# Optimization experiments

Hardware: AMD Instinct MI355X
Metric: run time of the kernel (lower is better)

## Reference

```python
import jax, jax.numpy as jnp
import numpy as np
import math

B, S, FDIM, D_MODEL, N_SCALES = 8, 2048, 64, 512, 5

def _layer_norm(h, g, b, eps=1e-5):
    mu = h.mean(-1, keepdims=True)
    var = h.var(-1, keepdims=True)
    return (h - mu) * jax.lax.rsqrt(var + eps) * g + b

def setup_inputs() -> dict:
    key = jax.random.key(0)
    ks = jax.random.split(key, 12)
    sc = lambda fan_in: 1.0 / np.sqrt(fan_in)
    inp = {
        'x': jax.random.normal(ks[0], (B, S, FDIM), dtype=jnp.float32),
        # relative_positional_encoding: Linear(3, d_model)
        'w_rel': jax.random.uniform(ks[1], (D_MODEL, 3), minval=-sc(3), maxval=sc(3), dtype=jnp.float32),
        'b_rel': jnp.zeros((D_MODEL,), jnp.float32),
        # event_encoding_projection: Linear(feature_dim, d_model)
        'w_proj': jax.random.uniform(ks[2], (D_MODEL, FDIM), minval=-sc(FDIM), maxval=sc(FDIM), dtype=jnp.float32),
        'b_proj': jnp.zeros((D_MODEL,), jnp.float32),
        'g1': jnp.ones((D_MODEL,), jnp.float32), 'bt1': jnp.zeros((D_MODEL,), jnp.float32),
        'g2': jnp.ones((D_MODEL,), jnp.float32), 'bt2': jnp.zeros((D_MODEL,), jnp.float32),
        'alpha': jnp.asarray(0.5, jnp.float32),
        'sigma_w': jnp.ones((1,), jnp.float32),
        'wq': jax.random.uniform(ks[3], (FDIM, FDIM), minval=-sc(FDIM), maxval=sc(FDIM), dtype=jnp.float32),
        'bq': jnp.zeros((FDIM,), jnp.float32),
        'wk': jax.random.uniform(ks[4], (FDIM, FDIM), minval=-sc(FDIM), maxval=sc(FDIM), dtype=jnp.float32),
        'bk': jnp.zeros((FDIM,), jnp.float32),
        'scale_w': jax.nn.softplus(jax.random.normal(ks[5], (N_SCALES,), dtype=jnp.float32)),
    }
    return inp

def reference(x, w_rel, b_rel, w_proj, b_proj, g1, bt1, g2, bt2, alpha, sigma_w, wq, bq, wk, bk, scale_w):
    bsz, seq_len, fdim = x.shape
    # distances / energies are the first two physical feature channels
    distances = x[:, :, 0]
    energies = x[:, :, 1]
    dd_list, de_list, wd_list = [], [], []
    for scale in range(1, N_SCALES + 1):  # static small loop (clamp(5,3,15).round()=5)
        dd = distances[:, :-scale] - distances[:, scale:]
        de = energies[:, :-scale] - energies[:, scale:]
        wd = scale_w[scale - 1] * jnp.exp(-jnp.abs(dd) / (2.0 ** scale))
        pad = ((0, 0), (scale, 0))
        dd_list.append(jnp.pad(dd, pad))
        de_list.append(jnp.pad(de, pad))
        wd_list.append(jnp.pad(wd, pad))
    delta_distances = jnp.stack(dd_list, axis=-1)   # [B,S,n_scales]
    delta_energies = jnp.stack(de_list, axis=-1)
    weighted_distances = jnp.stack(wd_list, axis=-1)
    rel = jnp.stack([delta_distances, delta_energies, weighted_distances], axis=-1)  # [B,S,n_scales,3]
    rel_enc = (jnp.einsum('bsnt,dt->bsnd', rel, w_rel) + b_rel).sum(axis=2)  # [B,S,D]
    rel_enc = _layer_norm(rel_enc, g1, bt1)

    # hybrid similarity
    x_norm = x / jnp.maximum(jnp.linalg.norm(x, axis=-1, keepdims=True), 1e-12)
    cos_sim = (jnp.einsum('bsd,btd->bst', x_norm, x_norm) + 1.0) / 2.0
    # pairwise euclidean distance via gram trick (avoids B*S*S*d intermediate)
    sq = jnp.sum(x * x, axis=-1)                                  # [B,S]
    d2 = sq[:, :, None] + sq[:, None, :] - 2.0 * jnp.einsum('bsd,btd->bst', x, x)
    d2 = jnp.maximum(d2, 0.0)
    euclid = jnp.where(d2 > 0, jnp.sqrt(jnp.maximum(d2, 1e-12)), 0.0)
    mean_dist = euclid.mean()
    std_dist = jnp.std(euclid, ddof=1)
    dev = euclid - mean_dist
    euclid = jnp.where(jnp.abs(dev) > 2 * std_dist, jnp.sign(dev) * (2 * std_dist) + mean_dist, euclid)
    euclid = (euclid - euclid.min()) / (euclid.max() - euclid.min() + 1e-6)
    a = jax.nn.sigmoid(alpha)
    hybrid = a * cos_sim + (1 - a) * (1 - euclid)

    sigma = jax.nn.softplus(sigma_w) + 0.001          # [1]
    q = jnp.einsum('bsf,gf->bsg', x, wq) + bq
    k = jnp.einsum('bsf,gf->bsg', x, wk) + bk
    scores = jnp.einsum('bsg,btg->bst', q, k) / math.sqrt(fdim)
    weights = jax.nn.softmax(scores, axis=-1)
    E = weights * jnp.exp(-hybrid / (2.0 * sigma[0] ** 2))
    pe_event = jnp.einsum('bst,btf->bsf', E, x)
    pe_proj = jnp.einsum('bsf,df->bsd', pe_event, w_proj) + b_proj
    pe_proj = _layer_norm(pe_proj, g2, bt2)
    return rel_enc + pe_proj
```

## Files before the change

kernel.cpp:

```cpp
#include <hip/hip_runtime.h>
#include <math.h>

#define B_ 8
#define S_ 2048
#define F_ 64
#define D_ 512
#define NS_ 5
#define BS_ (B_*S_)
#define NTILE_ 528
#define NPART_ (NTILE_*B_)

typedef unsigned short u16;
typedef __attribute__((ext_vector_type(8))) short short8;
typedef __attribute__((ext_vector_type(4))) float f32x4;

#define WS_SQ    0
#define WS_REL   (BS_)
#define WS_PE    (4*BS_)
#define WS_WPB   (WS_PE + 20480)
#define WS_STATS (68*BS_)
#define US_BASE_FLOATS (68*BS_ + 16)
#define US_XB 0
#define US_QB (BS_*64)
#define US_KB (2*BS_*64)
#define US_XT (3*BS_*64)

#define MFMA16(a,b,c) __builtin_amdgcn_mfma_f32_16x16x32_bf16(a,b,c,0,0,0)

__device__ __forceinline__ u16 f2bf(float f){
  unsigned u = __float_as_uint(f);
  return (u16)((u + 0x7FFFu + ((u>>16)&1u)) >> 16);
}
__device__ __forceinline__ int swz_phys(int row, int c){ return row*64 + (((c ^ (row & 15))) << 2); }

__global__ __launch_bounds__(256) void k1_prep(
    const float* __restrict__ x, const float* __restrict__ wq, const float* __restrict__ bq,
    const float* __restrict__ wk, const float* __restrict__ bk,
    const float* __restrict__ scale_w, const float* __restrict__ wp,
    float* __restrict__ ws, u16* __restrict__ usb, u16* __restrict__ wpb)
{
  __shared__ __align__(16) float xl[16*68];
  __shared__ __align__(16) float wql[4096];
  __shared__ __align__(16) float wkl[4096];
  int tid = threadIdx.x, lane = tid & 63, wv = tid >> 6;
  int row0 = blockIdx.x * 16;
  {
    int r = tid >> 4, c = tid & 15;
    *(float4*)(xl + r*68 + c*4) = *(const float4*)(x + (size_t)(row0 + r)*F_ + c*4);
  }
  for (int i = 0; i < 4; ++i){
    int idx = tid + i*256;
    int g = idx >> 4, c = idx & 15;
    float4 v = *(const float4*)(wq + g*F_ + c*4);
    int pb = swz_phys(g, c);
    wql[pb]=v.x; wql[pb+1]=v.y; wql[pb+2]=v.z; wql[pb+3]=v.w;
    float4 u = *(const float4*)(wk + g*F_ + c*4);
    wkl[pb]=u.x; wkl[pb+1]=u.y; wkl[pb+2]=u.z; wkl[pb+3]=u.w;
  }
  if (blockIdx.x < 32){
    int i2 = (blockIdx.x*256 + tid)*4;
    float4 v = *(const float4*)(wp + i2);
    uint2 pk2;
    pk2.x = (unsigned)f2bf(v.x) | ((unsigned)f2bf(v.y)<<16);
    pk2.y = (unsigned)f2bf(v.z) | ((unsigned)f2bf(v.w)<<16);
    *(uint2*)(wpb + i2) = pk2;
  }
  __syncthreads();
  int g = lane;
  int swl = g & 15;
  float qa[4], ka[4];
  #pragma unroll
  for (int j=0;j<4;++j){ qa[j]=bq[g]; ka[j]=bk[g]; }
  #pragma unroll
  for (int c=0;c<16;++c){
    float4 wqv = *(const float4*)(wql + g*64 + ((c ^ swl)<<2));
    float4 wkv = *(const float4*)(wkl + g*64 + ((c ^ swl)<<2));
    #pragma unroll
    for (int j=0;j<4;++j){
      float4 xv = *(const float4*)(xl + (wv*4+j)*68 + c*4);
      qa[j] += xv.x*wqv.x + xv.y*wqv.y + xv.z*wqv.z + xv.w*wqv.w;
      ka[j] += xv.x*wkv.x + xv.y*wkv.y + xv.z*wkv.z + xv.w*wkv.w;
    }
  }
  #pragma unroll
  for (int j=0;j<4;++j){
    int rg = row0 + wv*4 + j;
    usb[US_QB + (size_t)rg*64 + g] = f2bf(qa[j]);
    usb[US_KB + (size_t)rg*64 + g] = f2bf(ka[j]);
  }
  #pragma unroll
  for (int j=0;j<4;++j){
    int r = wv*4 + j;
    float v = xl[r*68 + lane];
    float s = v*v;
    for (int o=32;o;o>>=1) s += __shfl_xor(s, o, 64);
    if (lane == 0) ws[WS_SQ + row0 + r] = s;
  }
  #pragma unroll
  for (int j=0;j<4;++j){
    int r = wv*4 + j;
    int rg = row0 + r;
    int b = rg >> 11, s_loc = rg & (S_-1);
    float d0 = xl[r*68 + 0], e0 = xl[r*68 + 1];
    float dd = 0.f, de = 0.f, wd = 0.f;
    int n = lane + 1;
    if (lane < NS_ && s_loc >= n){
      const float* xp = x + ((size_t)(b*S_ + s_loc - n))*F_;
      float dp_ = xp[0], ep = xp[1];
      dd = dp_ - d0;
      de = ep - e0;
      wd = scale_w[lane] * __expf(-fabsf(dd) * (1.0f/(float)(1<<n)));
    }
    for (int o=4;o;o>>=1){
      dd += __shfl_down(dd, o, 64);
      de += __shfl_down(de, o, 64);
      wd += __shfl_down(wd, o, 64);
    }
    if (lane == 0){
      ws[WS_REL + rg*3+0] = dd;
      ws[WS_REL + rg*3+1] = de;
      ws[WS_REL + rg*3+2] = wd;
    }
  }
  {
    int r = tid >> 4, cb = (tid & 15)*4;
    unsigned w0 = (unsigned)f2bf(xl[r*68+cb])   | ((unsigned)f2bf(xl[r*68+cb+1])<<16);
    unsigned w1 = (unsigned)f2bf(xl[r*68+cb+2]) | ((unsigned)f2bf(xl[r*68+cb+3])<<16);
    uint2 pk; pk.x = w0; pk.y = w1;
    *(uint2*)(usb + US_XB + (size_t)(row0+r)*64 + cb) = pk;
  }
  {
    int f = tid & 63, rg4 = (tid >> 6)*4;
    unsigned wa = (unsigned)f2bf(xl[(rg4+0)*68+f]) | ((unsigned)f2bf(xl[(rg4+1)*68+f])<<16);
    unsigned wb = (unsigned)f2bf(xl[(rg4+2)*68+f]) | ((unsigned)f2bf(xl[(rg4+3)*68+f])<<16);
    uint2 pk; pk.x = wa; pk.y = wb;
    int bb = row0 >> 11;
    int tloc = (row0 & (S_-1)) + rg4;
    *(uint2*)(usb + US_XT + (size_t)bb*64*2048 + (size_t)f*2048 + tloc) = pk;
  }
}

__global__ __launch_bounds__(256) void k2_stats(const u16* __restrict__ us, float* __restrict__ ws)
{
  __shared__ __align__(16) u16 Xls[4096];
  __shared__ float sqs_l[64], sqt_l[64];
  __shared__ float rsum[4], rss[4], rmn[4], rmx[4];
  int tid = threadIdx.x, lane = tid & 63, wv = tid >> 6;
  int lg = lane >> 4, lc = lane & 15;
  int b = blockIdx.y;
  int rem = blockIdx.x, i = 0;
  while (rem >= 32 - i){ rem -= 32 - i; ++i; }
  int j = i + rem;
  int s0 = i*64, t0 = j*64;
  size_t rb = (size_t)b * S_;
  const u16* xb = us + US_XB;
  #pragma unroll
  for (int p2=0;p2<2;++p2){
    int slot = tid + p2*256;
    int row = slot>>3, pc = slot&7, lcn = pc ^ (row&7);
    ((short8*)Xls)[slot] = *(const short8*)(xb + (rb + t0 + row)*64 + lcn*8);
  }
  if (tid < 64) sqs_l[tid] = ws[WS_SQ + rb + s0 + tid];
  else if (tid < 128) sqt_l[tid-64] = ws[WS_SQ + rb + t0 + (tid-64)];
  short8 a0 = *(const short8*)(xb + (rb + s0 + wv*16 + lc)*64 + lg*8);
  short8 a1 = *(const short8*)(xb + (rb + s0 + wv*16 + lc)*64 + 32 + lg*8);
  __syncthreads();
  f32x4 acc[4];
  #pragma unroll
  for (int t=0;t<4;++t){ acc[t][0]=0.f; acc[t][1]=0.f; acc[t][2]=0.f; acc[t][3]=0.f; }
  #pragma unroll
  for (int ts=0; ts<4; ++ts){
    int rowb = ts*16 + lc;
    int sw = rowb & 7;
    short8 b0 = *(const short8*)(Xls + rowb*64 + ((lg ^ sw)<<3));
    short8 b1 = *(const short8*)(Xls + rowb*64 + (((4+lg) ^ sw)<<3));
    acc[ts] = MFMA16(a0, b0, acc[ts]);
    acc[ts] = MFMA16(a1, b1, acc[ts]);
  }
  float sq_s[4];
  #pragma unroll
  for (int r=0;r<4;++r) sq_s[r] = sqs_l[wv*16 + lg*4 + r];
  float lsum=0.f, lss=0.f, lmn=3.4e38f, lmx=-3.4e38f;
  #pragma unroll
  for (int ts=0; ts<4; ++ts){
    float sqt = sqt_l[ts*16 + lc];
    #pragma unroll
    for (int r=0;r<4;++r){
      float gg = acc[ts][r];
      float d2 = sq_s[r] + sqt - 2.f*gg;
      d2 = fmaxf(d2, 0.f);
      float eu = d2 > 0.f ? sqrtf(d2) : 0.f;
      lsum += eu; lss += eu*eu;
      lmn = fminf(lmn, eu); lmx = fmaxf(lmx, eu);
    }
  }
  for (int o=32;o;o>>=1){
    lsum += __shfl_xor(lsum, o, 64);
    lss  += __shfl_xor(lss, o, 64);
    lmn = fminf(lmn, __shfl_xor(lmn, o, 64));
    lmx = fmaxf(lmx, __shfl_xor(lmx, o, 64));
  }
  if (lane == 0){ rsum[wv]=lsum; rss[wv]=lss; rmn[wv]=lmn; rmx[wv]=lmx; }
  __syncthreads();
  if (tid == 0){
    float bs=0.f, bss=0.f, bmn=3.4e38f, bmx=-3.4e38f;
    for (int w2=0;w2<4;++w2){ bs+=rsum[w2]; bss+=rss[w2]; bmn=fminf(bmn,rmn[w2]); bmx=fmaxf(bmx,rmx[w2]); }
    float wgt = (i==j) ? 1.f : 2.f;
    float* part = ws + WS_PE;
    int bid = blockIdx.y * NTILE_ + blockIdx.x;
    part[bid]           = bs*wgt;
    part[NPART_ + bid]  = bss*wgt;
    part[2*NPART_ + bid]= bmn;
    part[3*NPART_ + bid]= bmx;
  }
}

__global__ __launch_bounds__(256) void k3_fin(const float* __restrict__ alpha,
                                              const float* __restrict__ sigma_w, float* ws){
  __shared__ double ssm[256], sss[256];
  __shared__ float smn[256], smx[256];
  int tid = threadIdx.x;
  const float* part = ws + WS_PE;
  double s = 0.0, ss = 0.0;
  float mn = 3.4e38f, mx = -3.4e38f;
  for (int i2 = tid; i2 < NPART_; i2 += 256){
    s  += (double)part[i2];
    ss += (double)part[NPART_ + i2];
    mn = fminf(mn, part[2*NPART_ + i2]);
    mx = fmaxf(mx, part[3*NPART_ + i2]);
  }
  ssm[tid]=s; sss[tid]=ss; smn[tid]=mn; smx[tid]=mx;
  __syncthreads();
  for (int st = 128; st; st >>= 1){
    if (tid < st){
      ssm[tid] += ssm[tid+st];
      sss[tid] += sss[tid+st];
      smn[tid] = fminf(smn[tid], smn[tid+st]);
      smx[tid] = fmaxf(smx[tid], smx[tid+st]);
    }
    __syncthreads();
  }
  if (tid == 0){
    double N = (double)B_*S_*S_;
    double sum = ssm[0], sumsq = sss[0];
    double mean = sum/N;
    double var  = (sumsq - sum*sum/N) / (N - 1.0);
    float stdv = (float)sqrt(fmax(var, 0.0));
    float m = (float)mean;
    float lo = m - 2.f*stdv, hi = m + 2.f*stdv;
    float cmn = fminf(fmaxf(smn[0], lo), hi);
    float cmx = fminf(fmaxf(smx[0], lo), hi);
    float invr = 1.f/(cmx - cmn + 1e-6f);
    float a = 1.f/(1.f + expf(-alpha[0]));
    float oma = 1.f - a;
    float swv = sigma_w[0];
    float sp = (swv > 20.f) ? swv : log1pf(expf(swv));
    float sg = sp + 0.001f;
    float efac = -0.5f/(sg*sg);
    float cg = efac*a*0.5f;
    float ce = -efac*oma*invr;
    float cc = efac*(a*0.5f + oma + oma*invr*cmn);
    float* p = ws + WS_STATS + 8;
    p[0]=lo; p[1]=hi; p[2]=cg; p[3]=ce; p[4]=cc;
  }
}

__global__ __launch_bounds__(512) void k4_flash(const u16* __restrict__ us,
                                                float* __restrict__ ws, u16* qout)
{
  __shared__ __align__(16) u16 SMEM[16384];
  __shared__ float sqt_l[64], invt_l[64];
  __shared__ float zb[4][2][16];
  u16* Kls  = SMEM;
  u16* Xls  = SMEM + 4096;
  u16* XTls = SMEM + 8192;
  u16* elp  = SMEM + 12288;
  int tid = threadIdx.x, lane = tid & 63, wv = tid >> 6;
  int lg = lane >> 4, lc = lane & 15;
  int ssub = wv >> 1, th = wv & 1;
  int b = blockIdx.y;
  size_t rb = (size_t)b * S_;
  int s0 = blockIdx.x * 64;
  const u16* xb = us + US_XB;
  const u16* qb = us + US_QB;
  const u16* kb = us + US_KB;
  const u16* xt = us + US_XT + (size_t)b*64*2048;
  int srow = s0 + ssub*16 + lc;
  short8 qf0 = *(const short8*)(qb + (rb+srow)*64 + lg*8);
  short8 qf1 = *(const short8*)(qb + (rb+srow)*64 + 32 + lg*8);
  short8 xf0 = *(const short8*)(xb + (rb+srow)*64 + lg*8);
  short8 xf1 = *(const short8*)(xb + (rb+srow)*64 + 32 + lg*8);
  const float* prm = ws + WS_STATS + 8;
  float lo=prm[0], hi=prm[1], cg=prm[2], ce=prm[3], cc=prm[4];
  float sq_s[4], cgis[4];
  #pragma unroll
  for (int r=0;r<4;++r){
    float s = ws[WS_SQ + rb + s0 + ssub*16 + lg*4 + r];
    sq_s[r] = s;
    cgis[r] = cg / fmaxf(sqrtf(s), 1e-12f);
  }
  f32x4 pe[4];
  #pragma unroll
  for (int t=0;t<4;++t){ pe[t][0]=0.f; pe[t][1]=0.f; pe[t][2]=0.f; pe[t][3]=0.f; }
  float zrun[4];
  #pragma unroll
  for (int r=0;r<4;++r) zrun[r]=0.f;

  for (int t0 = 0; t0 < S_; t0 += 64){
    {
      int slot = tid;
      int row = slot>>3, pc = slot&7, lcn = pc ^ (row&7);
      ((short8*)Kls)[slot]  = *(const short8*)(kb + (rb + t0 + row)*64 + lcn*8);
      ((short8*)Xls)[slot]  = *(const short8*)(xb + (rb + t0 + row)*64 + lcn*8);
      ((short8*)XTls)[slot] = *(const short8*)(xt + (size_t)row*2048 + t0 + lcn*8);
    }
    if (tid < 64){
      float s = ws[WS_SQ + rb + t0 + tid];
      sqt_l[tid] = s;
      invt_l[tid] = 1.f / fmaxf(sqrtf(s), 1e-12f);
    }
    __syncthreads();
    f32x4 ga[2], sa[2];
    #pragma unroll
    for (int t=0;t<2;++t){ ga[t][0]=0.f; ga[t][1]=0.f; ga[t][2]=0.f; ga[t][3]=0.f;
                           sa[t][0]=0.f; sa[t][1]=0.f; sa[t][2]=0.f; sa[t][3]=0.f; }
    #pragma unroll
    for (int ts=0; ts<2; ++ts){
      int rowb = (2*th+ts)*16 + lc;
      int sw = rowb & 7;
      short8 bk0 = *(const short8*)(Kls + rowb*64 + ((lg ^ sw)<<3));
      short8 bx0 = *(const short8*)(Xls + rowb*64 + ((lg ^ sw)<<3));
      sa[ts] = MFMA16(qf0, bk0, sa[ts]);
      ga[ts] = MFMA16(xf0, bx0, ga[ts]);
      short8 bk1 = *(const short8*)(Kls + rowb*64 + (((4+lg) ^ sw)<<3));
      short8 bx1 = *(const short8*)(Xls + rowb*64 + (((4+lg) ^ sw)<<3));
      sa[ts] = MFMA16(qf1, bk1, sa[ts]);
      ga[ts] = MFMA16(xf1, bx1, ga[ts]);
    }
    #pragma unroll
    for (int ts=0; ts<2; ++ts){
      int col = (2*th+ts)*16 + lc;
      float sqt = sqt_l[col], invt = invt_l[col];
      #pragma unroll
      for (int r=0;r<4;++r){
        float gg = ga[ts][r];
        float d2 = fmaxf(__builtin_fmaf(-2.f, gg, sq_s[r] + sqt), 0.f);
        float eu = fminf(fmaxf(sqrtf(d2), lo), hi);
        float arg = __builtin_fmaf(cgis[r]*invt, gg, cc);
        arg = __builtin_fmaf(ce, eu, arg);
        float s8 = __builtin_fmaf(sa[ts][r], 0.125f, -8.f);
        float p = __expf(s8);
        float pH = __expf(arg + s8);
        zrun[r] += p;
        int rowl = lg*4 + r;
        int phys = rowl*64 + ((((col>>3) ^ (rowl&7)))<<3) + (col&7);
        elp[ssub*1024 + phys] = f2bf(pH);
      }
    }
    {
      int swA = lc & 7;
      short8 Ae = *(const short8*)(elp + ssub*1024 + lc*64 + (((4*th + lg) ^ swA)<<3));
      #pragma unroll
      for (int fs=0; fs<4; ++fs){
        int rowf = fs*16 + lc;
        short8 Bx = *(const short8*)(XTls + rowf*64 + (((4*th + lg) ^ (rowf&7))<<3));
        pe[fs] = MFMA16(Ae, Bx, pe[fs]);
      }
    }
    __syncthreads();
  }
  #pragma unroll
  for (int r=0;r<4;++r){
    float z = zrun[r];
    z += __shfl_xor(z, 1, 64);
    z += __shfl_xor(z, 2, 64);
    z += __shfl_xor(z, 4, 64);
    z += __shfl_xor(z, 8, 64);
    if (lc == r) zb[ssub][th][lg*4+r] = z;
  }
  __syncthreads();
  float* tmp = (float*)SMEM;
  if (th == 1){
    #pragma unroll
    for (int fs=0; fs<4; ++fs)
      #pragma unroll
      for (int r=0;r<4;++r)
        tmp[ssub*1024 + (lg*4+r)*64 + fs*16 + lc] = pe[fs][r];
  }
  __syncthreads();
  if (th == 0){
    float zi[4];
    #pragma unroll
    for (int r=0;r<4;++r) zi[r] = 1.f / (zb[ssub][0][lg*4+r] + zb[ssub][1][lg*4+r]);
    #pragma unroll
    for (int fs=0; fs<4; ++fs)
      #pragma unroll
      for (int r=0;r<4;++r){
        float v = pe[fs][r] + tmp[ssub*1024 + (lg*4+r)*64 + fs*16 + lc];
        qout[US_QB + (rb + s0 + ssub*16 + lg*4 + r)*64 + fs*16 + lc] = f2bf(v * zi[r]);
      }
  }
}

__global__ __launch_bounds__(256) void k5_final(
    const float* __restrict__ w_rel, const float* __restrict__ b_rel,
    const float* __restrict__ b_proj,
    const float* __restrict__ g1, const float* __restrict__ bt1,
    const float* __restrict__ g2, const float* __restrict__ bt2,
    const float* __restrict__ ws, const u16* __restrict__ usb,
    const u16* __restrict__ wpb, float* __restrict__ out)
{
  __shared__ __align__(16) float res[16*512];
  __shared__ float rsl[48];
  __shared__ float g1l[512], b1l[512], g2l[512], b2l[512], brl[512], wrl[1536];
  int tid = threadIdx.x, lane = tid & 63, wv = tid >> 6;
  int lg = lane >> 4, lc = lane & 15;
  int row0 = blockIdx.x * 16;
  const u16* peb = usb + US_QB;
  short8 a0 = *(const short8*)(peb + (size_t)(row0+lc)*64 + lg*8);
  short8 a1 = *(const short8*)(peb + (size_t)(row0+lc)*64 + 32 + lg*8);
  if (tid < 48) rsl[tid] = ws[WS_REL + row0*3 + tid];
  for (int i = tid; i < 512; i += 256){
    g1l[i]=g1[i]; b1l[i]=bt1[i]; g2l[i]=g2[i]; b2l[i]=bt2[i]; brl[i]=b_rel[i];
  }
  for (int i = tid; i < 1536; i += 256) wrl[i] = w_rel[i];
  int wc0 = wv*128;
  #pragma unroll
  for (int cg=0; cg<8; ++cg){
    int d = wc0 + cg*16 + lc;
    short8 b0 = *(const short8*)(wpb + (size_t)d*64 + lg*8);
    short8 b1 = *(const short8*)(wpb + (size_t)d*64 + 32 + lg*8);
    f32x4 acc = {0.f,0.f,0.f,0.f};
    acc = MFMA16(a0, b0, acc);
    acc = MFMA16(a1, b1, acc);
    float bp = b_proj[d];
    #pragma unroll
    for (int r=0;r<4;++r) res[(lg*4+r)*512 + d] = acc[r] + bp;
  }
  __syncthreads();
  #pragma unroll
  for (int j=0;j<4;++j){
    int r = wv*4 + j;
    int rg = row0 + r;
    float s1=0.f, q1=0.f;
    float vals[8];
    #pragma unroll
    for (int i=0;i<8;++i){ float v = res[r*512 + i*64 + lane]; vals[i]=v; s1+=v; q1+=v*v; }
    for (int o=32;o;o>>=1){ s1 += __shfl_xor(s1,o,64); q1 += __shfl_xor(q1,o,64); }
    float mu1 = s1*(1.f/512.f);
    float var1 = q1*(1.f/512.f) - mu1*mu1;
    float rsg1 = rsqrtf(fmaxf(var1, 0.f) + 1e-5f);
    float c0 = rsl[r*3+0], c1 = rsl[r*3+1], c2 = rsl[r*3+2];
    float rv[8]; float s2=0.f, q2=0.f;
    #pragma unroll
    for (int i=0;i<8;++i){
      int d = i*64 + lane;
      float v = c0*wrl[d*3+0] + c1*wrl[d*3+1] + c2*wrl[d*3+2] + 5.f*brl[d];
      rv[i]=v; s2+=v; q2+=v*v;
    }
    for (int o=32;o;o>>=1){ s2 += __shfl_xor(s2,o,64); q2 += __shfl_xor(q2,o,64); }
    float mu2 = s2*(1.f/512.f);
    float var2 = q2*(1.f/512.f) - mu2*mu2;
    float rsg2 = rsqrtf(fmaxf(var2, 0.f) + 1e-5f);
    #pragma unroll
    for (int i=0;i<8;++i){
      int d = i*64 + lane;
      float o1 = (vals[i]-mu1)*rsg1*g2l[d] + b2l[d];
      float o2 = (rv[i]-mu2)*rsg2*g1l[d] + b1l[d];
      out[(size_t)rg*512 + d] = o1 + o2;
    }
  }
}

extern "C" void kernel_launch(void* const* d_in, const int* in_sizes, int n_in,
                              void* d_out, int out_size, void* d_ws, size_t ws_size,
                              hipStream_t stream)
{
  const float* x      = (const float*)d_in[0];
  const float* w_rel  = (const float*)d_in[1];
  const float* b_rel  = (const float*)d_in[2];
  const float* w_proj = (const float*)d_in[3];
  const float* b_proj = (const float*)d_in[4];
  const float* g1     = (const float*)d_in[5];
  const float* bt1    = (const float*)d_in[6];
  const float* g2     = (const float*)d_in[7];
  const float* bt2    = (const float*)d_in[8];
  const float* alpha  = (const float*)d_in[9];
  const float* sigma_w= (const float*)d_in[10];
  const float* wq     = (const float*)d_in[11];
  const float* bq     = (const float*)d_in[12];
  const float* wk     = (const float*)d_in[13];
  const float* bk     = (const float*)d_in[14];
  const float* scale_w= (const float*)d_in[15];
  float* wsf = (float*)d_ws;
  u16*  usb = (u16*)(wsf + US_BASE_FLOATS);
  u16*  wpb = (u16*)(wsf + WS_WPB);
  float* out = (float*)d_out;

  hipLaunchKernelGGL(k1_prep, dim3(BS_/16), dim3(256), 0, stream,
                     x, wq, bq, wk, bk, scale_w, w_proj, wsf, usb, wpb);
  hipLaunchKernelGGL(k2_stats, dim3(NTILE_, B_), dim3(256), 0, stream, usb, wsf);
  hipLaunchKernelGGL(k3_fin, dim3(1), dim3(256), 0, stream, alpha, sigma_w, wsf);
  hipLaunchKernelGGL(k4_flash, dim3(S_/64, B_), dim3(512), 0, stream, usb, wsf, usb);
  hipLaunchKernelGGL(k5_final, dim3(BS_/16), dim3(256), 0, stream,
                     w_rel, b_rel, b_proj, g1, bt1, g2, bt2, wsf, usb, wpb, out);
}
```

Measured before the change: 216.7 us.

## Split flash kernel over key dimension into two halves, combine partials in final kernel

The attention-like k4 kernel now launches a third grid dimension that splits the key range in two. Each half writes unnormalized fp32 partial sums and row normalizers into the output buffer, which serves as scratch. k5 then sums the two partials, normalizes, and converts to bf16 before the projection. This doubles block count from 256 to 512 to fill more CUs, at the cost of extra fp32 partial traffic and a combine step.

New measurement: 202.7 us. -6.5%, faster.

```diff
diff --git a/kernel.cpp b/kernel.cpp
--- a/kernel.cpp
+++ b/kernel.cpp
@@ -266,7 +266,8 @@
 }
 
 __global__ __launch_bounds__(512) void k4_flash(const u16* __restrict__ us,
-                                                float* __restrict__ ws, u16* qout)
+                                                const float* __restrict__ ws,
+                                                float* __restrict__ outsc)
 {
   __shared__ __align__(16) u16 SMEM[16384];
   __shared__ float sqt_l[64], invt_l[64];
@@ -279,6 +280,7 @@
   int lg = lane >> 4, lc = lane & 15;
   int ssub = wv >> 1, th = wv & 1;
   int b = blockIdx.y;
+  int h = blockIdx.z;
   size_t rb = (size_t)b * S_;
   int s0 = blockIdx.x * 64;
   const u16* xb = us + US_XB;
@@ -306,7 +308,8 @@
   #pragma unroll
   for (int r=0;r<4;++r) zrun[r]=0.f;
 
-  for (int t0 = 0; t0 < S_; t0 += 64){
+  int tbeg = h * (S_/2), tend = tbeg + (S_/2);
+  for (int t0 = tbeg; t0 < tend; t0 += 64){
     {
       int slot = tid;
       int row = slot>>3, pc = slot&7, lcn = pc ^ (row&7);
@@ -389,16 +392,17 @@
   }
   __syncthreads();
   if (th == 0){
-    float zi[4];
-    #pragma unroll
-    for (int r=0;r<4;++r) zi[r] = 1.f / (zb[ssub][0][lg*4+r] + zb[ssub][1][lg*4+r]);
+    size_t base = (((rb + s0) >> 4) + ssub) * 8192;
+    float* sc = outsc + base + (size_t)h*2048;
     #pragma unroll
     for (int fs=0; fs<4; ++fs)
       #pragma unroll
       for (int r=0;r<4;++r){
         float v = pe[fs][r] + tmp[ssub*1024 + (lg*4+r)*64 + fs*16 + lc];
-        qout[US_QB + (rb + s0 + ssub*16 + lg*4 + r)*64 + fs*16 + lc] = f2bf(v * zi[r]);
+        sc[(lg*4+r)*64 + fs*16 + lc] = v;
       }
+    if (lg == 0)
+      outsc[base + 4096 + h*16 + lc] = zb[ssub][0][lc] + zb[ssub][1][lc];
   }
 }
 
@@ -407,8 +411,7 @@
     const float* __restrict__ b_proj,
     const float* __restrict__ g1, const float* __restrict__ bt1,
     const float* __restrict__ g2, const float* __restrict__ bt2,
-    const float* __restrict__ ws, const u16* __restrict__ usb,
-    const u16* __restrict__ wpb, float* __restrict__ out)
+    const float* __restrict__ ws, const u16* __restrict__ wpb, float* out)
 {
   __shared__ __align__(16) float res[16*512];
   __shared__ float rsl[48];
@@ -416,9 +419,31 @@
   int tid = threadIdx.x, lane = tid & 63, wv = tid >> 6;
   int lg = lane >> 4, lc = lane & 15;
   int row0 = blockIdx.x * 16;
-  const u16* peb = usb + US_QB;
-  short8 a0 = *(const short8*)(peb + (size_t)(row0+lc)*64 + lg*8);
-  short8 a1 = *(const short8*)(peb + (size_t)(row0+lc)*64 + 32 + lg*8);
+  size_t base5 = (size_t)blockIdx.x * 8192;
+  float zi = 1.f / (out[base5 + 4096 + lc] + out[base5 + 4096 + 16 + lc]);
+  short8 a0, a1;
+  {
+    const float* p0 = out + base5 + (size_t)lc*64 + lg*8;
+    const float* p1 = p0 + 2048;
+    float4 u0 = *(const float4*)(p0);
+    float4 u1 = *(const float4*)(p0 + 4);
+    float4 v0 = *(const float4*)(p1);
+    float4 v1 = *(const float4*)(p1 + 4);
+    a0[0]=(short)f2bf((u0.x+v0.x)*zi); a0[1]=(short)f2bf((u0.y+v0.y)*zi);
+    a0[2]=(short)f2bf((u0.z+v0.z)*zi); a0[3]=(short)f2bf((u0.w+v0.w)*zi);
+    a0[4]=(short)f2bf((u1.x+v1.x)*zi); a0[5]=(short)f2bf((u1.y+v1.y)*zi);
+    a0[6]=(short)f2bf((u1.z+v1.z)*zi); a0[7]=(short)f2bf((u1.w+v1.w)*zi);
+    const float* q0 = p0 + 32;
+    const float* q1 = p1 + 32;
+    float4 w0 = *(const float4*)(q0);
+    float4 w1 = *(const float4*)(q0 + 4);
+    float4 y0 = *(const float4*)(q1);
+    float4 y1 = *(const float4*)(q1 + 4);
+    a1[0]=(short)f2bf((w0.x+y0.x)*zi); a1[1]=(short)f2bf((w0.y+y0.y)*zi);
+    a1[2]=(short)f2bf((w0.z+y0.z)*zi); a1[3]=(short)f2bf((w0.w+y0.w)*zi);
+    a1[4]=(short)f2bf((w1.x+y1.x)*zi); a1[5]=(short)f2bf((w1.y+y1.y)*zi);
+    a1[6]=(short)f2bf((w1.z+y1.z)*zi); a1[7]=(short)f2bf((w1.w+y1.w)*zi);
+  }
   if (tid < 48) rsl[tid] = ws[WS_REL + row0*3 + tid];
   for (int i = tid; i < 512; i += 256){
     g1l[i]=g1[i]; b1l[i]=bt1[i]; g2l[i]=g2[i]; b2l[i]=bt2[i]; brl[i]=b_rel[i];
@@ -426,8 +451,8 @@
   for (int i = tid; i < 1536; i += 256) wrl[i] = w_rel[i];
   int wc0 = wv*128;
   #pragma unroll
-  for (int cg=0; cg<8; ++cg){
-    int d = wc0 + cg*16 + lc;
+  for (int cgi=0; cgi<8; ++cgi){
+    int d = wc0 + cgi*16 + lc;
     short8 b0 = *(const short8*)(wpb + (size_t)d*64 + lg*8);
     short8 b1 = *(const short8*)(wpb + (size_t)d*64 + 32 + lg*8);
     f32x4 acc = {0.f,0.f,0.f,0.f};
@@ -501,7 +526,7 @@
                      x, wq, bq, wk, bk, scale_w, w_proj, wsf, usb, wpb);
   hipLaunchKernelGGL(k2_stats, dim3(NTILE_, B_), dim3(256), 0, stream, usb, wsf);
   hipLaunchKernelGGL(k3_fin, dim3(1), dim3(256), 0, stream, alpha, sigma_w, wsf);
-  hipLaunchKernelGGL(k4_flash, dim3(S_/64, B_), dim3(512), 0, stream, usb, wsf, usb);
+  hipLaunchKernelGGL(k4_flash, dim3(S_/64, B_, 2), dim3(512), 0, stream, usb, wsf, out);
   hipLaunchKernelGGL(k5_final, dim3(BS_/16), dim3(256), 0, stream,
-                     w_rel, b_rel, b_proj, g1, bt1, g2, bt2, wsf, usb, wpb, out);
-}
+                     w_rel, b_rel, b_proj, g1, bt1, g2, bt2, wsf, wpb, out);
+}
```

## Split flash kernel key range four ways and reduce partials in final kernel

Applied to the files above, without the earlier changes.

The attention-style k4_flash kernel now splits the key dimension into four chunks along a new grid z axis, so four times as many blocks run, each covering a quarter of the sequence. Each block writes unnormalized bf16 partial sums and partial normalizers into scratch space inside the output buffer. k5_final then sums the four partials, divides by the combined normalizer, and proceeds with the projection as before. The aim is to fix the low occupancy of the original 256-block launch of 512-thread blocks. The cost is extra partial traffic, a small reduction step, and a loss of precision from storing the partials in bf16.

New measurement: 203.1 us. 6.3% less time.

```diff
diff --git a/kernel.cpp b/kernel.cpp
--- a/kernel.cpp
+++ b/kernel.cpp
@@ -30,6 +30,9 @@
 __device__ __forceinline__ u16 f2bf(float f){
   unsigned u = __float_as_uint(f);
   return (u16)((u + 0x7FFFu + ((u>>16)&1u)) >> 16);
+}
+__device__ __forceinline__ float b2f(short s){
+  return __uint_as_float(((unsigned)(unsigned short)s) << 16);
 }
 __device__ __forceinline__ int swz_phys(int row, int c){ return row*64 + (((c ^ (row & 15))) << 2); }
 
@@ -266,7 +269,8 @@
 }
 
 __global__ __launch_bounds__(512) void k4_flash(const u16* __restrict__ us,
-                                                float* __restrict__ ws, u16* qout)
+                                                const float* __restrict__ ws,
+                                                float* __restrict__ outsc)
 {
   __shared__ __align__(16) u16 SMEM[16384];
   __shared__ float sqt_l[64], invt_l[64];
@@ -279,6 +283,7 @@
   int lg = lane >> 4, lc = lane & 15;
   int ssub = wv >> 1, th = wv & 1;
   int b = blockIdx.y;
+  int h = blockIdx.z;
   size_t rb = (size_t)b * S_;
   int s0 = blockIdx.x * 64;
   const u16* xb = us + US_XB;
@@ -306,7 +311,8 @@
   #pragma unroll
   for (int r=0;r<4;++r) zrun[r]=0.f;
 
-  for (int t0 = 0; t0 < S_; t0 += 64){
+  int tbeg = h * (S_/4), tend = tbeg + (S_/4);
+  for (int t0 = tbeg; t0 < tend; t0 += 64){
     {
       int slot = tid;
       int row = slot>>3, pc = slot&7, lcn = pc ^ (row&7);
@@ -389,16 +395,17 @@
   }
   __syncthreads();
   if (th == 0){
-    float zi[4];
-    #pragma unroll
-    for (int r=0;r<4;++r) zi[r] = 1.f / (zb[ssub][0][lg*4+r] + zb[ssub][1][lg*4+r]);
+    size_t rowblk = ((rb + (size_t)s0) >> 4) + ssub;
+    u16* scp = (u16*)outsc + rowblk*16384 + (size_t)h*1024;
     #pragma unroll
     for (int fs=0; fs<4; ++fs)
       #pragma unroll
       for (int r=0;r<4;++r){
         float v = pe[fs][r] + tmp[ssub*1024 + (lg*4+r)*64 + fs*16 + lc];
-        qout[US_QB + (rb + s0 + ssub*16 + lg*4 + r)*64 + fs*16 + lc] = f2bf(v * zi[r]);
+        scp[(lg*4+r)*64 + fs*16 + lc] = f2bf(v);
       }
+    if (lg == 0)
+      outsc[rowblk*8192 + 2048 + h*16 + lc] = zb[ssub][0][lc] + zb[ssub][1][lc];
   }
 }
 
@@ -407,8 +414,7 @@
     const float* __restrict__ b_proj,
     const float* __restrict__ g1, const float* __restrict__ bt1,
     const float* __restrict__ g2, const float* __restrict__ bt2,
-    const float* __restrict__ ws, const u16* __restrict__ usb,
-    const u16* __restrict__ wpb, float* __restrict__ out)
+    const float* __restrict__ ws, const u16* __restrict__ wpb, float* out)
 {
   __shared__ __align__(16) float res[16*512];
   __shared__ float rsl[48];
@@ -416,9 +422,29 @@
   int tid = threadIdx.x, lane = tid & 63, wv = tid >> 6;
   int lg = lane >> 4, lc = lane & 15;
   int row0 = blockIdx.x * 16;
-  const u16* peb = usb + US_QB;
-  short8 a0 = *(const short8*)(peb + (size_t)(row0+lc)*64 + lg*8);
-  short8 a1 = *(const short8*)(peb + (size_t)(row0+lc)*64 + 32 + lg*8);
+  size_t base5 = (size_t)blockIdx.x * 8192;
+  const u16* pb = (const u16*)out + (size_t)blockIdx.x * 16384;
+  float zi = 1.f / (out[base5+2048+lc] + out[base5+2048+16+lc]
+                  + out[base5+2048+32+lc] + out[base5+2048+48+lc]);
+  short8 a0, a1;
+  {
+    int off0 = lc*64 + lg*8;
+    short8 h0 = *(const short8*)(pb + off0);
+    short8 h1 = *(const short8*)(pb + 1024 + off0);
+    short8 h2 = *(const short8*)(pb + 2048 + off0);
+    short8 h3 = *(const short8*)(pb + 3072 + off0);
+    #pragma unroll
+    for (int e=0;e<8;++e)
+      a0[e] = (short)f2bf((b2f(h0[e]) + b2f(h1[e]) + b2f(h2[e]) + b2f(h3[e])) * zi);
+    int off1 = off0 + 32;
+    short8 j0 = *(const short8*)(pb + off1);
+    short8 j1 = *(const short8*)(pb + 1024 + off1);
+    short8 j2 = *(const short8*)(pb + 2048 + off1);
+    short8 j3 = *(const short8*)(pb + 3072 + off1);
+    #pragma unroll
+    for (int e=0;e<8;++e)
+      a1[e] = (short)f2bf((b2f(j0[e]) + b2f(j1[e]) + b2f(j2[e]) + b2f(j3[e])) * zi);
+  }
   if (tid < 48) rsl[tid] = ws[WS_REL + row0*3 + tid];
   for (int i = tid; i < 512; i += 256){
     g1l[i]=g1[i]; b1l[i]=bt1[i]; g2l[i]=g2[i]; b2l[i]=bt2[i]; brl[i]=b_rel[i];
@@ -426,8 +452,8 @@
   for (int i = tid; i < 1536; i += 256) wrl[i] = w_rel[i];
   int wc0 = wv*128;
   #pragma unroll
-  for (int cg=0; cg<8; ++cg){
-    int d = wc0 + cg*16 + lc;
+  for (int cgi=0; cgi<8; ++cgi){
+    int d = wc0 + cgi*16 + lc;
     short8 b0 = *(const short8*)(wpb + (size_t)d*64 + lg*8);
     short8 b1 = *(const short8*)(wpb + (size_t)d*64 + 32 + lg*8);
     f32x4 acc = {0.f,0.f,0.f,0.f};
@@ -501,7 +527,7 @@
                      x, wq, bq, wk, bk, scale_w, w_proj, wsf, usb, wpb);
   hipLaunchKernelGGL(k2_stats, dim3(NTILE_, B_), dim3(256), 0, stream, usb, wsf);
   hipLaunchKernelGGL(k3_fin, dim3(1), dim3(256), 0, stream, alpha, sigma_w, wsf);
-  hipLaunchKernelGGL(k4_flash, dim3(S_/64, B_), dim3(512), 0, stream, usb, wsf, usb);
+  hipLaunchKernelGGL(k4_flash, dim3(S_/64, B_, 4), dim3(512), 0, stream, usb, wsf, out);
   hipLaunchKernelGGL(k5_final, dim3(BS_/16), dim3(256), 0, stream,
-                     w_rel, b_rel, b_proj, g1, bt1, g2, bt2, wsf, usb, wpb, out);
-}
+                     w_rel, b_rel, b_proj, g1, bt1, g2, bt2, wsf, wpb, out);
+}
```
